# Performance work log

Measured on AMD Instinct MI355X. Metric: run time of the kernel, lower is better.

## Reference

```python
import jax, jax.numpy as jnp
import numpy as np

N_HEADS = 16


def build_bd3lm_mask(n, block_size, dtype):
    """BD3LM mask for concatenated [xt | x0] input of length 2n.
    0 = attend, finfo.min = masked. Shape (2n, 2n)."""
    idx = jnp.arange(2 * n)
    q_idx = idx[:, None]
    kv_idx = idx[None, :]
    x0_q = q_idx >= n
    x0_kv = kv_idx >= n
    block_q = jnp.where(x0_q, (q_idx - n) // block_size, q_idx // block_size)
    block_kv = jnp.where(x0_kv, (kv_idx - n) // block_size, kv_idx // block_size)
    block_diagonal = (block_q == block_kv) & (x0_q == x0_kv)
    offset_block_causal = (block_q > block_kv) & x0_kv & (~x0_q)
    block_causal = (block_q >= block_kv) & x0_kv & x0_q
    can_attend = block_diagonal | offset_block_causal | block_causal
    neg = jnp.finfo(dtype).min
    return jnp.where(can_attend, jnp.array(0, dtype), jnp.array(neg, dtype))


def setup_inputs() -> dict:
    key = jax.random.key(0)
    ks = jax.random.split(key, 5)
    B, T, D = 4, 2048, 1024  # T = 2*L, L = 1024
    s = 1.0 / np.sqrt(D)
    return {
        "x": jax.random.normal(ks[0], (B, T, D), jnp.float32),
        "Wq": jax.random.normal(ks[1], (D, D), jnp.float32) * s,
        "bq": jnp.zeros((D,), jnp.float32),
        "Wk": jax.random.normal(ks[2], (D, D), jnp.float32) * s,
        "bk": jnp.zeros((D,), jnp.float32),
        "Wv": jax.random.normal(ks[3], (D, D), jnp.float32) * s,
        "bv": jnp.zeros((D,), jnp.float32),
        "Wo": jax.random.normal(ks[4], (D, D), jnp.float32) * s,
        "bo": jnp.zeros((D,), jnp.float32),
        "block_size": 4,
    }


def reference(x, Wq, bq, Wk, bk, Wv, bv, Wo, bo, block_size):
    B, T, D = x.shape
    H = N_HEADS
    hd = D // H
    n = T // 2  # length of each copy in [xt | x0]
    mask = build_bd3lm_mask(n, block_size, x.dtype)  # (T, T)

    def split_heads(t):  # (B, T, D) -> (B, H, T, hd)
        return t.reshape(B, T, H, hd).transpose(0, 2, 1, 3)

    q = split_heads(x @ Wq + bq) * (hd ** -0.5)
    k = split_heads(x @ Wk + bk)
    v = split_heads(x @ Wv + bv)
    scores = jnp.einsum("bhqd,bhkd->bhqk", q, k) + mask[None, None]
    attn = jax.nn.softmax(scores, axis=-1)
    ctx = jnp.einsum("bhqk,bhkd->bhqd", attn, v)
    ctx = ctx.transpose(0, 2, 1, 3).reshape(B, T, D)
    return ctx @ Wo + bo
```

## Files before the change

### kernel.cpp

```cpp
#include <hip/hip_runtime.h>
#include <hip/hip_bf16.h>
#include <stdint.h>

typedef __hip_bfloat16 bf16;
typedef short v8s __attribute__((ext_vector_type(8)));
typedef float v4f __attribute__((ext_vector_type(4)));

#define TT   2048
#define DD   1024
#define HH   16
#define HDIM 64
#define NN   1024
#define MASKV (-1e9f)
#define QSCALE 0.18033688011112042f

#if __has_builtin(__builtin_amdgcn_exp2f)
#define EXP2F(x) __builtin_amdgcn_exp2f(x)
#else
#define EXP2F(x) exp2f(x)
#endif

__device__ __forceinline__ v4f mfma16x16x32(v8s a, v8s b, v4f c) {
    return __builtin_amdgcn_mfma_f32_16x16x32_bf16(a, b, c, 0, 0, 0);
}

#define GLDS16(lds, g)                                                          \
    __builtin_amdgcn_global_load_lds(                                           \
        (const __attribute__((address_space(1))) void*)(g),                     \
        (__attribute__((address_space(3))) void*)(lds), 16, 0, 0)

__device__ __forceinline__ bf16 f2b(float f) { return __float2bfloat16(f); }

__global__ __launch_bounds__(256) void cast_x(const float* __restrict__ x,
                                              bf16* __restrict__ xb)
{
    const size_t i = ((size_t)blockIdx.x * 256 + threadIdx.x) * 4;
    const float4 f = *(const float4*)(x + i);
    union { bf16 b[4]; uint64_t u; } cv;
    cv.b[0] = f2b(f.x); cv.b[1] = f2b(f.y); cv.b[2] = f2b(f.z); cv.b[3] = f2b(f.w);
    *(uint64_t*)(xb + i) = cv.u;
}

__global__ __launch_bounds__(256) void transpose_w(
    const float* __restrict__ w0, const float* __restrict__ w1,
    const float* __restrict__ w2, const float* __restrict__ w3,
    bf16* __restrict__ dst)
{
    __shared__ float tile[64][65];
    const float* src = (blockIdx.z == 0) ? w0 : (blockIdx.z == 1) ? w1
                      : (blockIdx.z == 2) ? w2 : w3;
    bf16* d = dst + (size_t)blockIdx.z * 1024 * 1024;
    const int r0 = blockIdx.y * 64, c0 = blockIdx.x * 64;
    const int tx = threadIdx.x, ty = threadIdx.y;
#pragma unroll
    for (int j = 0; j < 16; j++) {
        int r = ty + j * 4;
        tile[r][tx] = src[(size_t)(r0 + r) * 1024 + c0 + tx];
    }
    __syncthreads();
#pragma unroll
    for (int j = 0; j < 16; j++) {
        int r = ty + j * 4;
        d[(size_t)(c0 + r) * 1024 + r0 + tx] = f2b(tile[tx][r]);
    }
}

__global__ __launch_bounds__(256) void transpose_v(
    const bf16* __restrict__ vtmp, bf16* __restrict__ vt)
{
    __shared__ bf16 tile[64][66];
    const int bh = blockIdx.y, t0 = blockIdx.x * 64;
    const int tx = threadIdx.x, ty = threadIdx.y;
    const bf16* src = vtmp + (size_t)bh * TT * HDIM;
    bf16* dst = vt + (size_t)bh * HDIM * TT;
#pragma unroll
    for (int j = 0; j < 16; j++) {
        int r = ty + j * 4;
        tile[r][tx] = src[(size_t)(t0 + r) * HDIM + tx];
    }
    __syncthreads();
#pragma unroll
    for (int j = 0; j < 16; j++) {
        int r = ty + j * 4;
        dst[(size_t)r * TT + t0 + tx] = tile[tx][r];
    }
}

__global__ __launch_bounds__(256) void gemm_qkv(
    const bf16* __restrict__ A, const bf16* __restrict__ BT,
    const float* __restrict__ bq, const float* __restrict__ bk,
    const float* __restrict__ bv,
    bf16* __restrict__ qo, bf16* __restrict__ ko, bf16* __restrict__ vo)
{
    __shared__ __align__(16) bf16 At[128 * 32];
    __shared__ __align__(16) bf16 Bt[128 * 32];
    const int tid  = threadIdx.x;
    const int lane = tid & 63, wave = tid >> 6;
    const int quad = lane >> 4, c = lane & 15;
    const int wm = wave >> 1, wn = wave & 1;
    const int m0 = blockIdx.y * 128, n0 = blockIdx.x * 128;
    const int K = 1024;
    const int chunkrow = lane >> 2;
    const int kseg     = (lane & 3) * 8;

    v4f acc[4][4];
#pragma unroll
    for (int i = 0; i < 4; i++)
#pragma unroll
        for (int j = 0; j < 4; j++) acc[i][j] = (v4f){0.f, 0.f, 0.f, 0.f};

    for (int k0 = 0; k0 < K; k0 += 32) {
#pragma unroll
        for (int ch = 0; ch < 2; ch++) {
            const int chunk = wave * 2 + ch;
            const int row   = chunk * 16 + chunkrow;
            GLDS16(At + chunk * 512, A  + (size_t)(m0 + row) * K + k0 + kseg);
            GLDS16(Bt + chunk * 512, BT + (size_t)(n0 + row) * K + k0 + kseg);
        }
        asm volatile("s_waitcnt vmcnt(0)" ::: "memory");
        __syncthreads();

        v8s af[4], bfr[4];
#pragma unroll
        for (int mt = 0; mt < 4; mt++)
            af[mt] = *(const v8s*)(At + (wm * 64 + mt * 16 + c) * 32 + quad * 8);
#pragma unroll
        for (int nt = 0; nt < 4; nt++)
            bfr[nt] = *(const v8s*)(Bt + (wn * 64 + nt * 16 + c) * 32 + quad * 8);
#pragma unroll
        for (int mt = 0; mt < 4; mt++)
#pragma unroll
            for (int nt = 0; nt < 4; nt++)
                acc[mt][nt] = mfma16x16x32(af[mt], bfr[nt], acc[mt][nt]);
        __syncthreads();
    }

    const int type = n0 >> 10;
    bf16* o = (type == 0) ? qo : (type == 1) ? ko : vo;
    const float* bp = (type == 0) ? bq : (type == 1) ? bk : bv;
    const float scale = (type == 0) ? QSCALE : 1.0f;
    const int nbase = n0 & 1023;

#pragma unroll
    for (int mt = 0; mt < 4; mt++)
#pragma unroll
        for (int nt = 0; nt < 4; nt++) {
            const int within = nbase + wn * 64 + nt * 16 + c;
            const int h = within >> 6, d = within & 63;
            const float bias = bp[within];
#pragma unroll
            for (int r = 0; r < 4; r++) {
                const int row = m0 + wm * 64 + mt * 16 + quad * 4 + r;
                const int b_ = row >> 11, t = row & 2047;
                const int bh = b_ * HH + h;
                o[((size_t)bh * TT + t) * HDIM + d] =
                    f2b((acc[mt][nt][r] + bias) * scale);
            }
        }
}

__global__ __launch_bounds__(256) void gemm_out(
    const bf16* __restrict__ A, const bf16* __restrict__ BT,
    const float* __restrict__ bo, float* __restrict__ out)
{
    __shared__ __align__(16) bf16 At[128 * 32];
    __shared__ __align__(16) bf16 Bt[128 * 32];
    const int tid  = threadIdx.x;
    const int lane = tid & 63, wave = tid >> 6;
    const int quad = lane >> 4, c = lane & 15;
    const int wm = wave >> 1, wn = wave & 1;
    const int m0 = blockIdx.y * 128, n0 = blockIdx.x * 128;
    const int K = 1024;
    const int chunkrow = lane >> 2;
    const int kseg     = (lane & 3) * 8;

    v4f acc[4][4];
#pragma unroll
    for (int i = 0; i < 4; i++)
#pragma unroll
        for (int j = 0; j < 4; j++) acc[i][j] = (v4f){0.f, 0.f, 0.f, 0.f};

    for (int k0 = 0; k0 < K; k0 += 32) {
#pragma unroll
        for (int ch = 0; ch < 2; ch++) {
            const int chunk = wave * 2 + ch;
            const int row   = chunk * 16 + chunkrow;
            GLDS16(At + chunk * 512, A  + (size_t)(m0 + row) * K + k0 + kseg);
            GLDS16(Bt + chunk * 512, BT + (size_t)(n0 + row) * K + k0 + kseg);
        }
        asm volatile("s_waitcnt vmcnt(0)" ::: "memory");
        __syncthreads();

        v8s af[4], bfr[4];
#pragma unroll
        for (int mt = 0; mt < 4; mt++)
            af[mt] = *(const v8s*)(At + (wm * 64 + mt * 16 + c) * 32 + quad * 8);
#pragma unroll
        for (int nt = 0; nt < 4; nt++)
            bfr[nt] = *(const v8s*)(Bt + (wn * 64 + nt * 16 + c) * 32 + quad * 8);
#pragma unroll
        for (int mt = 0; mt < 4; mt++)
#pragma unroll
            for (int nt = 0; nt < 4; nt++)
                acc[mt][nt] = mfma16x16x32(af[mt], bfr[nt], acc[mt][nt]);
        __syncthreads();
    }

#pragma unroll
    for (int mt = 0; mt < 4; mt++)
#pragma unroll
        for (int nt = 0; nt < 4; nt++) {
            const int col = n0 + wn * 64 + nt * 16 + c;
            const float bias = bo[col];
#pragma unroll
            for (int r = 0; r < 4; r++) {
                const int row = m0 + wm * 64 + mt * 16 + quad * 4 + r;
                out[(size_t)row * 1024 + col] = acc[mt][nt][r] + bias;
            }
        }
}

__global__ __launch_bounds__(256, 4) void attn(
    const bf16* __restrict__ Q, const bf16* __restrict__ Kb,
    const bf16* __restrict__ VT, bf16* __restrict__ ctx,
    const int* __restrict__ bsp)
{
    __shared__ __align__(16) bf16 Kt[2][32 * 64];
    __shared__ __align__(16) bf16 Vt[2][64 * 32];
    __shared__ __align__(16) bf16 plds[4][2][16 * 32];

    const int bs = bsp[0];
    const float inv  = 1.0f / (float)bs;
    const float hinv = 0.5f * inv;
    const int tid = threadIdx.x, lane = tid & 63, wv = tid >> 6;
    const int quad = lane >> 4, c = lane & 15;
    const int bh = blockIdx.x & 63;
    const int j  = blockIdx.x >> 6;
    const int g_tbl[16] = {7,6,5,4, 0,1,2,3, 4,5,6,7, 3,2,1,0};
    const bool xt = j < 8;
    const int g  = g_tbl[j];
    const int q0g = (xt ? 0 : NN) + g * 128;

    const bf16* qp = Q  + (size_t)bh * TT * HDIM;
    const bf16* kp = Kb + (size_t)bh * TT * HDIM;
    const bf16* vp = VT + (size_t)bh * HDIM * TT;

    int d_lo = 0, nd = 0, nf = 0, b_lo = 0, nb = 0;
    if (xt) {
        d_lo = (bs * (q0g / bs)) & ~31;
        const int d_hi = min((bs * ((q0g + 127) / bs) + bs + 31) & ~31, NN);
        nd = (d_hi - d_lo) >> 5;
        const int f = bs * (q0g / bs);
        nf = f >> 5;
        b_lo = NN + (nf << 5);
        const int b_hi = NN + min((bs * ((q0g + 127) / bs) + 31) & ~31, NN);
        nb = (b_hi > b_lo) ? (b_hi - b_lo) >> 5 : 0;
    } else {
        const int q0l = q0g - NN;
        const int f = min(bs * (q0l / bs) + bs, NN);
        nf = f >> 5;
        b_lo = NN + (nf << 5);
        const int b_hi = NN + min((bs * ((q0l + 127) / bs) + bs + 31) & ~31, NN);
        nb = (b_hi > b_lo) ? (b_hi - b_lo) >> 5 : 0;
    }
    const int nc = nd + nf + nb;

    float bqv[2][4];
#pragma unroll
    for (int t = 0; t < 2; t++)
#pragma unroll
        for (int r = 0; r < 4; r++) {
            const int qrow = q0g + wv * 32 + t * 16 + quad * 4 + r;
            const int qloc = xt ? qrow : qrow - NN;
            bqv[t][r] = floorf(fmaf((float)qloc, inv, hinv));
        }

    v8s aq[2][2];
#pragma unroll
    for (int t = 0; t < 2; t++) {
        const int rowb = q0g + wv * 32 + t * 16;
        aq[t][0] = *(const v8s*)(qp + (size_t)(rowb + c) * HDIM + quad * 8);
        aq[t][1] = *(const v8s*)(qp + (size_t)(rowb + c) * HDIM + 32 + quad * 8);
    }

    v4f O[2][4];
#pragma unroll
    for (int t = 0; t < 2; t++)
#pragma unroll
        for (int dt = 0; dt < 4; dt++) O[t][dt] = (v4f){0.f, 0.f, 0.f, 0.f};
    float lr[2][4] = {{0.f,0.f,0.f,0.f},{0.f,0.f,0.f,0.f}};

    const int klrow = lane >> 3, ks8 = lane & 7;
    const bf16* kSrc0 = kp + (size_t)(wv * 8 + klrow) * HDIM + ((ks8 ^ klrow) << 3);
    const int vlrow = lane >> 2, vs8 = lane & 3;
    const bf16* vSrc0 = vp + (size_t)(wv * 16 + vlrow) * TT + ((vs8 ^ (vlrow & 3)) << 3);

    auto kb_of = [&](int i, int& kb, int& type) {
        if (i < nd)           { kb = d_lo + (i << 5);             type = 1; }
        else if (i < nd + nf) { kb = NN + ((i - nd) << 5);        type = 0; }
        else                  { kb = b_lo + ((i - nd - nf) << 5); type = xt ? 2 : 3; }
    };
    auto stage = [&](int i) {
        int kb, ty; kb_of(i, kb, ty);
        const int sel = i & 1;
        GLDS16(&Kt[sel][wv * 512], kSrc0 + (size_t)kb * HDIM);
        GLDS16(&Vt[sel][wv * 512], vSrc0 + kb);
    };

    stage(0);
    asm volatile("s_waitcnt vmcnt(0)" ::: "memory");
    asm volatile("s_barrier" ::: "memory");

    const int xk = c & 7, xv = c & 3;
    const int pquad = quad << 3;
#pragma unroll 1
    for (int i = 0; i < nc; i++) {
        int kb, type; kb_of(i, kb, type);
        const int sel = i & 1;
        const bf16* Kl = Kt[sel];
        const bf16* Vl = Vt[sel];

        const v8s k0a = *(const v8s*)(Kl + c * 64        + ((quad       ^ xk) << 3));
        const v8s k0b = *(const v8s*)(Kl + c * 64        + (((quad ^ 4) ^ xk) << 3));
        const v8s k1a = *(const v8s*)(Kl + (16 + c) * 64 + ((quad       ^ xk) << 3));
        const v8s k1b = *(const v8s*)(Kl + (16 + c) * 64 + (((quad ^ 4) ^ xk) << 3));
        v8s vf[4];
#pragma unroll
        for (int dt = 0; dt < 4; dt++)
            vf[dt] = *(const v8s*)(Vl + (dt * 16 + c) * 32 + ((quad ^ xv) << 3));

        if (i + 1 < nc) stage(i + 1);

        float bkA = 0.f, bkB = 0.f;
        if (type) {
            const int off = (type == 1) ? 0 : NN;
            bkA = floorf(fmaf((float)(kb + c - off),      inv, hinv));
            bkB = floorf(fmaf((float)(kb + 16 + c - off), inv, hinv));
        }

#pragma unroll
        for (int t = 0; t < 2; t++) {
            v4f Sa = (v4f){0.f, 0.f, 0.f, 0.f};
            v4f Sb = (v4f){0.f, 0.f, 0.f, 0.f};
            Sa = mfma16x16x32(aq[t][0], k0a, Sa);
            Sa = mfma16x16x32(aq[t][1], k0b, Sa);
            Sb = mfma16x16x32(aq[t][0], k1a, Sb);
            Sb = mfma16x16x32(aq[t][1], k1b, Sb);
            bf16* pw = &plds[wv][t][(quad * 4) * 32];
#pragma unroll
            for (int r = 0; r < 4; r++) {
                float sa = Sa[r], sb = Sb[r];
                if (type == 1) {
                    if (bkA != bqv[t][r]) sa = MASKV;
                    if (bkB != bqv[t][r]) sb = MASKV;
                } else if (type == 2) {
                    if (!(bkA < bqv[t][r])) sa = MASKV;
                    if (!(bkB < bqv[t][r])) sb = MASKV;
                } else if (type == 3) {
                    if (!(bkA <= bqv[t][r])) sa = MASKV;
                    if (!(bkB <= bqv[t][r])) sb = MASKV;
                }
                const float pa = EXP2F(sa);
                const float pb = EXP2F(sb);
                lr[t][r] += pa + pb;
                pw[r * 32 + (c ^ pquad)]        = f2b(pa);
                pw[r * 32 + ((c + 16) ^ pquad)] = f2b(pb);
            }
        }
        asm volatile("s_waitcnt lgkmcnt(0)" ::: "memory");
#pragma unroll
        for (int t = 0; t < 2; t++) {
            const v8s pf = *(const v8s*)(&plds[wv][t][c * 32 +
                                        ((quad ^ ((c >> 2) & 3)) << 3)]);
#pragma unroll
            for (int dt = 0; dt < 4; dt++)
                O[t][dt] = mfma16x16x32(pf, vf[dt], O[t][dt]);
        }

        asm volatile("s_waitcnt vmcnt(0)" ::: "memory");
        asm volatile("s_barrier" ::: "memory");
    }

    const int b_ = bh >> 4, h = bh & 15;
#pragma unroll
    for (int t = 0; t < 2; t++)
#pragma unroll
        for (int r = 0; r < 4; r++) {
            float s = lr[t][r];
#pragma unroll
            for (int off = 1; off < 16; off <<= 1) s += __shfl_xor(s, off);
            const float invl = 1.0f / fmaxf(s, 1e-30f);
            const int trow = q0g + wv * 32 + t * 16 + quad * 4 + r;
#pragma unroll
            for (int dt = 0; dt < 4; dt++)
                ctx[((size_t)(b_ * TT + trow)) * DD + h * 64 + dt * 16 + c] =
                    f2b(O[t][dt][r] * invl);
        }
}

extern "C" void kernel_launch(void* const* d_in, const int* in_sizes, int n_in,
                              void* d_out, int out_size, void* d_ws, size_t ws_size,
                              hipStream_t stream)
{
    const float* x  = (const float*)d_in[0];
    const float* Wq = (const float*)d_in[1];
    const float* bq = (const float*)d_in[2];
    const float* Wk = (const float*)d_in[3];
    const float* bk = (const float*)d_in[4];
    const float* Wv = (const float*)d_in[5];
    const float* bv = (const float*)d_in[6];
    const float* Wo = (const float*)d_in[7];
    const float* bo = (const float*)d_in[8];
    const int*  bsp = (const int*)d_in[9];
    float* out = (float*)d_out;

    bf16* ws    = (bf16*)d_ws;
    bf16* xb    = ws;
    bf16* wqkvT = xb + 8388608;
    bf16* woT   = wqkvT + 3 * 1024 * 1024;
    bf16* qbuf  = woT + 1024 * 1024;
    bf16* kbuf  = qbuf + 8388608;
    bf16* vtmp  = kbuf + 8388608;
    bf16* vt    = vtmp + 8388608;
    bf16* ctx   = xb;

    cast_x<<<8192, 256, 0, stream>>>(x, xb);
    transpose_w<<<dim3(16, 16, 4), dim3(64, 4), 0, stream>>>(Wq, Wk, Wv, Wo, wqkvT);
    gemm_qkv<<<dim3(24, 64), 256, 0, stream>>>(xb, wqkvT, bq, bk, bv,
                                               qbuf, kbuf, vtmp);
    transpose_v<<<dim3(32, 64), dim3(64, 4), 0, stream>>>(vtmp, vt);
    attn<<<1024, 256, 0, stream>>>(qbuf, kbuf, vt, ctx, bsp);
    gemm_out<<<dim3(8, 64), 256, 0, stream>>>(ctx, woT, bo, out);
}
```

Before: 249.3 us.

## Rewrite QKV and output GEMMs with 256x128 double-buffered pipelined core

Replaces the simple 128x128, K=32 GEMM loop used by the QKV and output projections with a shared 256x128 tile core. The new core runs 512 threads, uses K=64 stages with XOR-swizzled LDS, and double-buffers the tiles so global-to-LDS loads for the next stage overlap the MFMA work. It also adds s_setprio around the MFMA bursts and remaps block ids so consecutive blocks share operand tiles in cache. The aim is to hide memory latency and raise MFMA utilisation in the projection GEMMs, at the cost of more LDS per block, higher register pressure and fragile manual vmcnt accounting.

New measurement: 244.6 us. Within noise of the previous version (-1.9%).

```diff
diff --git a/kernel.cpp b/kernel.cpp
--- a/kernel.cpp
+++ b/kernel.cpp
@@ -86,54 +86,120 @@
     }
 }
 
-__global__ __launch_bounds__(256) void gemm_qkv(
+__device__ __forceinline__ void gemm_core_256x128(
+    const bf16* __restrict__ A, const bf16* __restrict__ BT,
+    const int m0, const int n0, const int K,
+    bf16* __restrict__ As, bf16* __restrict__ Bs,
+    v4f (&acc)[8][2])
+{
+    const int tid  = threadIdx.x;
+    const int lane = tid & 63, wv = tid >> 6;
+    const int quad = lane >> 4, c = lane & 15;
+    const int wm = wv >> 2, wn = wv & 3;
+    const int c7 = c & 7;
+    const int NT = K >> 6;
+
+    const int rloc = wv * 8 + (lane >> 3);
+    const int gsw  = ((lane & 7) ^ ((lane >> 3) & 7)) << 3;
+    const bf16* aSrc = A  + (size_t)(m0 + rloc) * K + gsw;
+    const bf16* bSrc = BT + (size_t)(n0 + rloc) * K + gsw;
+
+#pragma unroll
+    for (int i = 0; i < 8; i++)
+#pragma unroll
+        for (int j = 0; j < 2; j++) acc[i][j] = (v4f){0.f, 0.f, 0.f, 0.f};
+
+    auto stageA = [&](bf16* dst, int j, int kt) {
+        const int mo = ((j & 1) << 7) | ((j >> 1) << 6);
+        GLDS16(dst + (j * 64 + wv * 8) * 64, aSrc + (size_t)mo * K + kt * 64);
+    };
+    auto stageB = [&](bf16* dst, int j, int kt) {
+        GLDS16(dst + (j * 64 + wv * 8) * 64, bSrc + (size_t)(j << 6) * K + kt * 64);
+    };
+
+    stageB(Bs, 0, 0); stageB(Bs, 1, 0);
+    stageA(As, 0, 0); stageA(As, 1, 0); stageA(As, 2, 0); stageA(As, 3, 0);
+    asm volatile("s_waitcnt vmcnt(2)" ::: "memory");
+    asm volatile("s_barrier" ::: "memory");
+
+#pragma unroll 1
+    for (int kt = 0; kt < NT; ++kt) {
+        bf16* Ac = As + (kt & 1) * 16384;
+        bf16* Bc = Bs + (kt & 1) * 8192;
+        bf16* An = As + ((kt & 1) ^ 1) * 16384;
+        bf16* Bn = Bs + ((kt & 1) ^ 1) * 8192;
+        const int ktn = (kt + 1 < NT) ? kt + 1 : kt;
+
+        v8s bfr[2][2];
+#pragma unroll
+        for (int nt = 0; nt < 2; nt++)
+#pragma unroll
+            for (int kh = 0; kh < 2; kh++)
+                bfr[nt][kh] = *(const v8s*)(Bc + (wn * 32 + nt * 16 + c) * 64
+                                            + (((kh * 4 + quad) ^ c7) << 3));
+        v8s af[4][2];
+#pragma unroll
+        for (int mt = 0; mt < 4; mt++)
+#pragma unroll
+            for (int kh = 0; kh < 2; kh++)
+                af[mt][kh] = *(const v8s*)(Ac + (wm * 64 + mt * 16 + c) * 64
+                                           + (((kh * 4 + quad) ^ c7) << 3));
+        stageB(Bn, 0, ktn); stageB(Bn, 1, ktn); stageA(An, 0, ktn);
+        asm volatile("s_barrier" ::: "memory");
+        __builtin_amdgcn_s_setprio(1);
+#pragma unroll
+        for (int mt = 0; mt < 4; mt++)
+#pragma unroll
+            for (int nt = 0; nt < 2; nt++) {
+                acc[mt][nt] = mfma16x16x32(af[mt][0], bfr[nt][0], acc[mt][nt]);
+                acc[mt][nt] = mfma16x16x32(af[mt][1], bfr[nt][1], acc[mt][nt]);
+            }
+        __builtin_amdgcn_s_setprio(0);
+        asm volatile("s_waitcnt vmcnt(3)" ::: "memory");
+        asm volatile("s_barrier" ::: "memory");
+
+#pragma unroll
+        for (int mt = 0; mt < 4; mt++)
+#pragma unroll
+            for (int kh = 0; kh < 2; kh++)
+                af[mt][kh] = *(const v8s*)(Ac + (128 + wm * 64 + mt * 16 + c) * 64
+                                           + (((kh * 4 + quad) ^ c7) << 3));
+        stageA(An, 1, ktn); stageA(An, 2, ktn); stageA(An, 3, ktn);
+        asm volatile("s_barrier" ::: "memory");
+        __builtin_amdgcn_s_setprio(1);
+#pragma unroll
+        for (int mt = 0; mt < 4; mt++)
+#pragma unroll
+            for (int nt = 0; nt < 2; nt++) {
+                acc[4 + mt][nt] = mfma16x16x32(af[mt][0], bfr[nt][0], acc[4 + mt][nt]);
+                acc[4 + mt][nt] = mfma16x16x32(af[mt][1], bfr[nt][1], acc[4 + mt][nt]);
+            }
+        __builtin_amdgcn_s_setprio(0);
+        asm volatile("s_waitcnt vmcnt(2)" ::: "memory");
+        asm volatile("s_barrier" ::: "memory");
+    }
+}
+
+__global__ __launch_bounds__(512, 2) void gemm_qkv(
     const bf16* __restrict__ A, const bf16* __restrict__ BT,
     const float* __restrict__ bq, const float* __restrict__ bk,
     const float* __restrict__ bv,
     bf16* __restrict__ qo, bf16* __restrict__ ko, bf16* __restrict__ vo)
 {
-    __shared__ __align__(16) bf16 At[128 * 32];
-    __shared__ __align__(16) bf16 Bt[128 * 32];
+    __shared__ __align__(16) bf16 As[2 * 256 * 64];
+    __shared__ __align__(16) bf16 Bs[2 * 128 * 64];
+    const int id  = blockIdx.x;
+    const int fid = (id & 7) * 96 + (id >> 3);
+    const int by  = fid / 24, bx = fid - by * 24;
+    const int m0  = by * 256, n0 = bx * 128;
+
+    v4f acc[8][2];
+    gemm_core_256x128(A, BT, m0, n0, 1024, As, Bs, acc);
+
     const int tid  = threadIdx.x;
-    const int lane = tid & 63, wave = tid >> 6;
+    const int lane = tid & 63, wv = tid >> 6;
     const int quad = lane >> 4, c = lane & 15;
-    const int wm = wave >> 1, wn = wave & 1;
-    const int m0 = blockIdx.y * 128, n0 = blockIdx.x * 128;
-    const int K = 1024;
-    const int chunkrow = lane >> 2;
-    const int kseg     = (lane & 3) * 8;
-
-    v4f acc[4][4];
-#pragma unroll
-    for (int i = 0; i < 4; i++)
-#pragma unroll
-        for (int j = 0; j < 4; j++) acc[i][j] = (v4f){0.f, 0.f, 0.f, 0.f};
-
-    for (int k0 = 0; k0 < K; k0 += 32) {
-#pragma unroll
-        for (int ch = 0; ch < 2; ch++) {
-            const int chunk = wave * 2 + ch;
-            const int row   = chunk * 16 + chunkrow;
-            GLDS16(At + chunk * 512, A  + (size_t)(m0 + row) * K + k0 + kseg);
-            GLDS16(Bt + chunk * 512, BT + (size_t)(n0 + row) * K + k0 + kseg);
-        }
-        asm volatile("s_waitcnt vmcnt(0)" ::: "memory");
-        __syncthreads();
-
-        v8s af[4], bfr[4];
-#pragma unroll
-        for (int mt = 0; mt < 4; mt++)
-            af[mt] = *(const v8s*)(At + (wm * 64 + mt * 16 + c) * 32 + quad * 8);
-#pragma unroll
-        for (int nt = 0; nt < 4; nt++)
-            bfr[nt] = *(const v8s*)(Bt + (wn * 64 + nt * 16 + c) * 32 + quad * 8);
-#pragma unroll
-        for (int mt = 0; mt < 4; mt++)
-#pragma unroll
-            for (int nt = 0; nt < 4; nt++)
-                acc[mt][nt] = mfma16x16x32(af[mt], bfr[nt], acc[mt][nt]);
-        __syncthreads();
-    }
+    const int wm = wv >> 2, wn = wv & 3;
 
     const int type = n0 >> 10;
     bf16* o = (type == 0) ? qo : (type == 1) ? ko : vo;
@@ -142,15 +208,15 @@
     const int nbase = n0 & 1023;
 
 #pragma unroll
-    for (int mt = 0; mt < 4; mt++)
-#pragma unroll
-        for (int nt = 0; nt < 4; nt++) {
-            const int within = nbase + wn * 64 + nt * 16 + c;
+    for (int mt = 0; mt < 8; mt++)
+#pragma unroll
+        for (int nt = 0; nt < 2; nt++) {
+            const int within = nbase + wn * 32 + nt * 16 + c;
             const int h = within >> 6, d = within & 63;
             const float bias = bp[within];
 #pragma unroll
             for (int r = 0; r < 4; r++) {
-                const int row = m0 + wm * 64 + mt * 16 + quad * 4 + r;
+                const int row = m0 + wm * 128 + mt * 16 + quad * 4 + r;
                 const int b_ = row >> 11, t = row & 2047;
                 const int bh = b_ * HH + h;
                 o[((size_t)bh * TT + t) * HDIM + d] =
@@ -159,62 +225,34 @@
         }
 }
 
-__global__ __launch_bounds__(256) void gemm_out(
+__global__ __launch_bounds__(512, 2) void gemm_out(
     const bf16* __restrict__ A, const bf16* __restrict__ BT,
     const float* __restrict__ bo, float* __restrict__ out)
 {
-    __shared__ __align__(16) bf16 At[128 * 32];
-    __shared__ __align__(16) bf16 Bt[128 * 32];
+    __shared__ __align__(16) bf16 As[2 * 256 * 64];
+    __shared__ __align__(16) bf16 Bs[2 * 128 * 64];
+    const int id  = blockIdx.x;
+    const int fid = (id & 7) * 32 + (id >> 3);
+    const int by  = fid >> 3, bx = fid & 7;
+    const int m0  = by * 256, n0 = bx * 128;
+
+    v4f acc[8][2];
+    gemm_core_256x128(A, BT, m0, n0, 1024, As, Bs, acc);
+
     const int tid  = threadIdx.x;
-    const int lane = tid & 63, wave = tid >> 6;
+    const int lane = tid & 63, wv = tid >> 6;
     const int quad = lane >> 4, c = lane & 15;
-    const int wm = wave >> 1, wn = wave & 1;
-    const int m0 = blockIdx.y * 128, n0 = blockIdx.x * 128;
-    const int K = 1024;
-    const int chunkrow = lane >> 2;
-    const int kseg     = (lane & 3) * 8;
-
-    v4f acc[4][4];
-#pragma unroll
-    for (int i = 0; i < 4; i++)
-#pragma unroll
-        for (int j = 0; j < 4; j++) acc[i][j] = (v4f){0.f, 0.f, 0.f, 0.f};
-
-    for (int k0 = 0; k0 < K; k0 += 32) {
-#pragma unroll
-        for (int ch = 0; ch < 2; ch++) {
-            const int chunk = wave * 2 + ch;
-            const int row   = chunk * 16 + chunkrow;
-            GLDS16(At + chunk * 512, A  + (size_t)(m0 + row) * K + k0 + kseg);
-            GLDS16(Bt + chunk * 512, BT + (size_t)(n0 + row) * K + k0 + kseg);
-        }
-        asm volatile("s_waitcnt vmcnt(0)" ::: "memory");
-        __syncthreads();
-
-        v8s af[4], bfr[4];
-#pragma unroll
-        for (int mt = 0; mt < 4; mt++)
-            af[mt] = *(const v8s*)(At + (wm * 64 + mt * 16 + c) * 32 + quad * 8);
-#pragma unroll
-        for (int nt = 0; nt < 4; nt++)
-            bfr[nt] = *(const v8s*)(Bt + (wn * 64 + nt * 16 + c) * 32 + quad * 8);
-#pragma unroll
-        for (int mt = 0; mt < 4; mt++)
-#pragma unroll
-            for (int nt = 0; nt < 4; nt++)
-                acc[mt][nt] = mfma16x16x32(af[mt], bfr[nt], acc[mt][nt]);
-        __syncthreads();
-    }
-
-#pragma unroll
-    for (int mt = 0; mt < 4; mt++)
-#pragma unroll
-        for (int nt = 0; nt < 4; nt++) {
-            const int col = n0 + wn * 64 + nt * 16 + c;
+    const int wm = wv >> 2, wn = wv & 3;
+
+#pragma unroll
+    for (int mt = 0; mt < 8; mt++)
+#pragma unroll
+        for (int nt = 0; nt < 2; nt++) {
+            const int col = n0 + wn * 32 + nt * 16 + c;
             const float bias = bo[col];
 #pragma unroll
             for (int r = 0; r < 4; r++) {
-                const int row = m0 + wm * 64 + mt * 16 + quad * 4 + r;
+                const int row = m0 + wm * 128 + mt * 16 + quad * 4 + r;
                 out[(size_t)row * 1024 + col] = acc[mt][nt][r] + bias;
             }
         }
@@ -426,9 +464,8 @@
 
     cast_x<<<8192, 256, 0, stream>>>(x, xb);
     transpose_w<<<dim3(16, 16, 4), dim3(64, 4), 0, stream>>>(Wq, Wk, Wv, Wo, wqkvT);
-    gemm_qkv<<<dim3(24, 64), 256, 0, stream>>>(xb, wqkvT, bq, bk, bv,
-                                               qbuf, kbuf, vtmp);
+    gemm_qkv<<<768, 512, 0, stream>>>(xb, wqkvT, bq, bk, bv, qbuf, kbuf, vtmp);
     transpose_v<<<dim3(32, 64), dim3(64, 4), 0, stream>>>(vtmp, vt);
     attn<<<1024, 256, 0, stream>>>(qbuf, kbuf, vt, ctx, bsp);
-    gemm_out<<<dim3(8, 64), 256, 0, stream>>>(ctx, woT, bo, out);
-}
+    gemm_out<<<256, 512, 0, stream>>>(ctx, woT, bo, out);
+}
```
